# Kernel optimization log

Hardware: AMD Instinct MI355X
Metric: run time of the kernel (lower is better)

## Reference

```python
import jax, jax.numpy as jnp
import numpy as np
import math

N_EMBD = 1024
N_HEAD = 16
HEAD_DIM = N_EMBD // N_HEAD
SCALE = 1.0 / math.sqrt(HEAD_DIM)


def setup_inputs() -> dict:
    key = jax.random.key(0)
    ks = jax.random.split(key, 5)
    B, S = 1, 4096
    std = 0.02
    x = jax.random.normal(ks[0], (B, S, N_EMBD), dtype=jnp.float32)
    # Linear weights stored as [in, out] (transposed vs torch storage; same math)
    w_qkv = jax.random.normal(ks[1], (N_EMBD, 3 * N_EMBD), dtype=jnp.float32) * std
    b_qkv = jnp.zeros((3 * N_EMBD,), dtype=jnp.float32)
    w_out = jax.random.normal(ks[2], (N_EMBD, N_EMBD), dtype=jnp.float32) * std
    b_out = jnp.zeros((N_EMBD,), dtype=jnp.float32)
    return {"x": x, "w_qkv": w_qkv, "b_qkv": b_qkv, "w_out": w_out, "b_out": b_out}


def reference(x, w_qkv, b_qkv, w_out, b_out):
    B, S, D = x.shape
    qkv = x @ w_qkv + b_qkv                      # [B, S, 3D]
    q, k, v = jnp.split(qkv, 3, axis=-1)
    # [B, H, S, d]
    q = q.reshape(B, S, N_HEAD, HEAD_DIM).transpose(0, 2, 1, 3)
    k = k.reshape(B, S, N_HEAD, HEAD_DIM).transpose(0, 2, 1, 3)
    v = v.reshape(B, S, N_HEAD, HEAD_DIM).transpose(0, 2, 1, 3)
    scores = jnp.einsum("bhqd,bhkd->bhqk", q, k) * SCALE  # [B, H, S, S]
    causal = jnp.tril(jnp.ones((S, S), dtype=bool))
    scores = jnp.where(causal, scores, -jnp.inf)
    attn = jax.nn.softmax(scores, axis=-1)
    out = jnp.einsum("bhqk,bhkd->bhqd", attn, v)  # [B, H, S, d]
    out = out.transpose(0, 2, 1, 3).reshape(B, S, D)
    return out @ w_out + b_out
```

## Files before the change

### kernel.cpp

```cpp
#include <hip/hip_runtime.h>
#include <hip/hip_bf16.h>
#include <cstdint>

typedef __bf16 bf16x8 __attribute__((ext_vector_type(8)));
typedef float  f32x4  __attribute__((ext_vector_type(4)));

#define S_LEN 4096
#define D_EMB 1024
#define N3    3072
#define HDIM  64

__device__ __forceinline__ unsigned short f2bf(float f) {
    union { unsigned int i; float f; } v; v.f = f;
    unsigned int i = v.i;
    return (unsigned short)((i + 0x7FFFu + ((i >> 16) & 1u)) >> 16);
}

__device__ __forceinline__ void async16(const void* g, void* l) {
    __builtin_amdgcn_global_load_lds(
        (const __attribute__((address_space(1))) unsigned int*)g,
        (__attribute__((address_space(3))) unsigned int*)l,
        16, 0, 0);
}

__global__ void convert_f32_bf16(const float* __restrict__ src,
                                 unsigned short* __restrict__ dst, int n8) {
    const int i = blockIdx.x * blockDim.x + threadIdx.x;
    if (i >= n8) return;
    float4 f0 = *(const float4*)&src[i * 8];
    float4 f1 = *(const float4*)&src[i * 8 + 4];
    union { uint4 q; unsigned short s[8]; } o;
    o.s[0]=f2bf(f0.x); o.s[1]=f2bf(f0.y); o.s[2]=f2bf(f0.z); o.s[3]=f2bf(f0.w);
    o.s[4]=f2bf(f1.x); o.s[5]=f2bf(f1.y); o.s[6]=f2bf(f1.z); o.s[7]=f2bf(f1.w);
    *(uint4*)&dst[i * 8] = o.q;
}

__global__ void transpose_f32_to_bf16(const float* __restrict__ src,
                                      unsigned short* __restrict__ dst,
                                      int R, int ld, int c0) {
    __shared__ float tile[32][33];
    const int tx = threadIdx.x, ty = threadIdx.y;
    const int r0 = blockIdx.y * 32, cc0 = blockIdx.x * 32;
    for (int i = 0; i < 32; i += 8)
        tile[ty + i][tx] = src[(size_t)(r0 + ty + i) * ld + c0 + cc0 + tx];
    __syncthreads();
    for (int i = 0; i < 32; i += 8)
        dst[(size_t)(cc0 + ty + i) * R + r0 + tx] = f2bf(tile[tx][ty + i]);
}

__global__ void transpose_bf16(const unsigned short* __restrict__ src,
                               unsigned short* __restrict__ dst,
                               int R, int ld, int c0) {
    __shared__ unsigned short tile[32][33];
    const int tx = threadIdx.x, ty = threadIdx.y;
    const int r0 = blockIdx.y * 32, cc0 = blockIdx.x * 32;
    for (int i = 0; i < 32; i += 8)
        tile[ty + i][tx] = src[(size_t)(r0 + ty + i) * ld + c0 + cc0 + tx];
    __syncthreads();
    for (int i = 0; i < 32; i += 8)
        dst[(size_t)(cc0 + ty + i) * R + r0 + tx] = tile[tx][ty + i];
}

template <bool OUT_F32>
__global__ __launch_bounds__(256) void gemm_bt_bias(
    const unsigned short* __restrict__ A,
    const unsigned short* __restrict__ BT,
    const float* __restrict__ bias,
    void* __restrict__ Cp,
    int M, int N, int K)
{
    __shared__ __align__(16) unsigned short As[128 * 32];
    __shared__ __align__(16) unsigned short Bs[128 * 32];
    const int tid  = threadIdx.x;
    const int wave = tid >> 6, lane = tid & 63;
    const int q4 = lane >> 4, l16 = lane & 15;
    const int m0 = blockIdx.y * 128, n0 = blockIdx.x * 128;
    const int wm = (wave >> 1) * 64, wn = (wave & 1) * 64;

    f32x4 acc[4][4] = {};

    const int srow = wave * 32 + (lane >> 2);
    const int scol = (lane & 3) * 8;

    for (int k0 = 0; k0 < K; k0 += 32) {
        __syncthreads();
        for (int i = 0; i < 2; ++i) {
            const int r = srow + i * 16;
            async16(A  + (size_t)(m0 + r) * K + k0 + scol,
                    &As[(wave * 32 + i * 16) * 32 + lane * 8]);
            async16(BT + (size_t)(n0 + r) * K + k0 + scol,
                    &Bs[(wave * 32 + i * 16) * 32 + lane * 8]);
        }
        __syncthreads();

        bf16x8 af[4], bfr[4];
        for (int mi = 0; mi < 4; ++mi)
            af[mi] = *(const bf16x8*)&As[(wm + mi * 16 + l16) * 32 + q4 * 8];
        for (int ni = 0; ni < 4; ++ni)
            bfr[ni] = *(const bf16x8*)&Bs[(wn + ni * 16 + l16) * 32 + q4 * 8];
        for (int mi = 0; mi < 4; ++mi)
            for (int ni = 0; ni < 4; ++ni)
                acc[mi][ni] = __builtin_amdgcn_mfma_f32_16x16x32_bf16(
                    af[mi], bfr[ni], acc[mi][ni], 0, 0, 0);
    }

    for (int ni = 0; ni < 4; ++ni) {
        const int col = n0 + wn + ni * 16 + l16;
        const float bv = bias[col];
        for (int mi = 0; mi < 4; ++mi) {
            const int row = m0 + wm + mi * 16 + q4 * 4;
            for (int r = 0; r < 4; ++r) {
                const float val = acc[mi][ni][r] + bv;
                if constexpr (OUT_F32)
                    ((float*)Cp)[(size_t)(row + r) * N + col] = val;
                else
                    ((unsigned short*)Cp)[(size_t)(row + r) * N + col] = f2bf(val);
            }
        }
    }
}

#define LDP 72
__global__ __launch_bounds__(256) void attn_flash(
    const unsigned short* __restrict__ qkv,
    const unsigned short* __restrict__ Vt,
    unsigned short* __restrict__ X2)
{
    __shared__ __align__(16) unsigned short Ks[64 * LDP];
    __shared__ __align__(16) unsigned short Vs[64 * LDP];
    __shared__ __align__(16) unsigned short Ps[4 * 16 * LDP];
    const int tid  = threadIdx.x;
    const int wave = tid >> 6, lane = tid & 63;
    const int q4 = lane >> 4, l16 = lane & 15;
    const int h  = blockIdx.y;

    const int x = blockIdx.x, hg = blockIdx.y >> 2;
    int qt;
    if      (hg == 0) qt = x;
    else if (hg == 1) qt = 63 - x;
    else if (hg == 2) qt = (x + 16) & 63;
    else              qt = (47 - x) & 63;
    const int q0 = qt * 64;

    bf16x8 aq[2];
    {
        const unsigned short* qp =
            qkv + (size_t)(q0 + wave * 16 + l16) * N3 + h * HDIM + q4 * 8;
        aq[0] = *(const bf16x8*)(qp);
        aq[1] = *(const bf16x8*)(qp + 32);
    }

    float l_part[4] = {0.f, 0.f, 0.f, 0.f};
    f32x4 o[4] = {};

    const int rr = tid >> 3;
    const int cc = (tid & 7) * 8;
    const int ntile = qt + 1;

    for (int t = 0; t < ntile; ++t) {
        const int kv0 = t * 64;
        uint4 kv_a = *(const uint4*)&qkv[(size_t)(kv0 + rr)      * N3 + D_EMB + h * HDIM + cc];
        uint4 kv_b = *(const uint4*)&qkv[(size_t)(kv0 + 32 + rr) * N3 + D_EMB + h * HDIM + cc];
        uint4 vt_a = *(const uint4*)&Vt [(size_t)(h * HDIM + rr)      * S_LEN + kv0 + cc];
        uint4 vt_b = *(const uint4*)&Vt [(size_t)(h * HDIM + 32 + rr) * S_LEN + kv0 + cc];
        __syncthreads();
        *(uint4*)&Ks[rr * LDP + cc]        = kv_a;
        *(uint4*)&Ks[(32 + rr) * LDP + cc] = kv_b;
        *(uint4*)&Vs[rr * LDP + cc]        = vt_a;
        *(uint4*)&Vs[(32 + rr) * LDP + cc] = vt_b;
        __syncthreads();

        f32x4 sacc[4] = {};
        for (int kk = 0; kk < 2; ++kk)
            for (int nt = 0; nt < 4; ++nt) {
                bf16x8 b = *(const bf16x8*)&Ks[(nt * 16 + l16) * LDP + kk * 32 + q4 * 8];
                sacc[nt] = __builtin_amdgcn_mfma_f32_16x16x32_bf16(
                    aq[kk], b, sacc[nt], 0, 0, 0);
            }

        const bool lastt = (t == ntile - 1);
        for (int r = 0; r < 4; ++r) {
            const int grow = q0 + wave * 16 + q4 * 4 + r;
            for (int nt = 0; nt < 4; ++nt) {
                float e = __expf(sacc[nt][r] * 0.125f);
                if (lastt && (kv0 + nt * 16 + l16 > grow)) e = 0.f;
                l_part[r] += e;
                Ps[wave * 16 * LDP + (q4 * 4 + r) * LDP + nt * 16 + l16] = f2bf(e);
            }
        }
        __asm__ volatile("s_waitcnt lgkmcnt(0)" ::: "memory");

        for (int kk = 0; kk < 2; ++kk) {
            bf16x8 pa = *(const bf16x8*)&Ps[wave * 16 * LDP + l16 * LDP + kk * 32 + q4 * 8];
            for (int dt = 0; dt < 4; ++dt) {
                bf16x8 vb = *(const bf16x8*)&Vs[(dt * 16 + l16) * LDP + kk * 32 + q4 * 8];
                o[dt] = __builtin_amdgcn_mfma_f32_16x16x32_bf16(pa, vb, o[dt], 0, 0, 0);
            }
        }
    }

    float linv[4];
    for (int r = 0; r < 4; ++r) {
        float l = l_part[r];
        for (int off = 1; off < 16; off <<= 1)
            l += __shfl_xor(l, off, 16);
        linv[r] = 1.f / l;
    }
    for (int dt = 0; dt < 4; ++dt)
        for (int r = 0; r < 4; ++r) {
            const int row = q0 + wave * 16 + q4 * 4 + r;
            X2[(size_t)row * D_EMB + h * HDIM + dt * 16 + l16] =
                f2bf(o[dt][r] * linv[r]);
        }
}

extern "C" void kernel_launch(void* const* d_in, const int* in_sizes, int n_in,
                              void* d_out, int out_size, void* d_ws, size_t ws_size,
                              hipStream_t stream) {
    const float* x     = (const float*)d_in[0];
    const float* w_qkv = (const float*)d_in[1];
    const float* b_qkv = (const float*)d_in[2];
    const float* w_out = (const float*)d_in[3];
    const float* b_out = (const float*)d_in[4];
    float* out = (float*)d_out;

    char* ws = (char*)d_ws;
    unsigned short* qkv   = (unsigned short*)(ws);
    unsigned short* wqkvT = (unsigned short*)(ws + 25165824);
    unsigned short* woutT = (unsigned short*)(ws + 31457280);
    unsigned short* Vt    = (unsigned short*)(ws + 33554432);
    unsigned short* X2    = (unsigned short*)(ws + 41943040);
    unsigned short* Xb    = X2;

    convert_f32_bf16<<<(4096 * 1024 / 8 + 255) / 256, 256, 0, stream>>>(
        x, Xb, 4096 * 1024 / 8);

    transpose_f32_to_bf16<<<dim3(3072 / 32, 1024 / 32), dim3(32, 8), 0, stream>>>(
        w_qkv, wqkvT, 1024, 3072, 0);
    transpose_f32_to_bf16<<<dim3(1024 / 32, 1024 / 32), dim3(32, 8), 0, stream>>>(
        w_out, woutT, 1024, 1024, 0);

    gemm_bt_bias<false><<<dim3(3072 / 128, 4096 / 128), 256, 0, stream>>>(
        Xb, wqkvT, b_qkv, qkv, 4096, 3072, 1024);

    transpose_bf16<<<dim3(1024 / 32, 4096 / 32), dim3(32, 8), 0, stream>>>(
        qkv, Vt, 4096, 3072, 2048);

    attn_flash<<<dim3(64, 16), 256, 0, stream>>>(qkv, Vt, X2);

    gemm_bt_bias<true><<<dim3(1024 / 128, 4096 / 128), 256, 0, stream>>>(
        X2, woutT, b_out, out, 4096, 1024, 1024);
}
```

Before: 248.4 us.

## Split KV tiles across waves with register-resident K/V and LDS reduction

Restructures the attention kernel so each wave handles all 64 query rows of the block but only every fourth KV tile. K and V fragments are loaded straight from global memory into registers, which removes the per-tile shared-memory staging and block barriers. The four waves' partial outputs and row sums are then combined through LDS in a tree reduction. The softmax scale and log2(e) are folded into Q in the QKV GEMM epilogue so exp2f can be used directly. The cost is much higher register pressure (64 accumulators per wave, launch_bounds 256,2), unbalanced tile counts across waves for small qt, and a loss of the previous head-group query-tile reordering.

```diff
diff --git a/kernel.cpp b/kernel.cpp
--- a/kernel.cpp
+++ b/kernel.cpp
@@ -9,6 +9,7 @@
 #define D_EMB 1024
 #define N3    3072
 #define HDIM  64
+#define QSCALE 0.180336884f
 
 __device__ __forceinline__ unsigned short f2bf(float f) {
     union { unsigned int i; float f; } v; v.f = f;
@@ -61,7 +62,7 @@
         dst[(size_t)(cc0 + ty + i) * R + r0 + tx] = tile[tx][ty + i];
 }
 
-template <bool OUT_F32>
+template <bool OUT_F32, bool SCALE_Q>
 __global__ __launch_bounds__(256) void gemm_bt_bias(
     const unsigned short* __restrict__ A,
     const unsigned short* __restrict__ BT,
@@ -107,10 +108,11 @@
     for (int ni = 0; ni < 4; ++ni) {
         const int col = n0 + wn + ni * 16 + l16;
         const float bv = bias[col];
+        const float sc = (SCALE_Q && col < 1024) ? QSCALE : 1.f;
         for (int mi = 0; mi < 4; ++mi) {
             const int row = m0 + wm + mi * 16 + q4 * 4;
             for (int r = 0; r < 4; ++r) {
-                const float val = acc[mi][ni][r] + bv;
+                const float val = (acc[mi][ni][r] + bv) * sc;
                 if constexpr (OUT_F32)
                     ((float*)Cp)[(size_t)(row + r) * N + col] = val;
                 else
@@ -120,98 +122,131 @@
     }
 }
 
-#define LDP 72
-__global__ __launch_bounds__(256) void attn_flash(
+#define PLD 72
+
+__global__ __launch_bounds__(256, 2) void attn_flash(
     const unsigned short* __restrict__ qkv,
     const unsigned short* __restrict__ Vt,
     unsigned short* __restrict__ X2)
 {
-    __shared__ __align__(16) unsigned short Ks[64 * LDP];
-    __shared__ __align__(16) unsigned short Vs[64 * LDP];
-    __shared__ __align__(16) unsigned short Ps[4 * 16 * LDP];
+    __shared__ __align__(16) unsigned char lds[4 * 64 * PLD * 2];
     const int tid  = threadIdx.x;
     const int wave = tid >> 6, lane = tid & 63;
     const int q4 = lane >> 4, l16 = lane & 15;
     const int h  = blockIdx.y;
-
-    const int x = blockIdx.x, hg = blockIdx.y >> 2;
-    int qt;
-    if      (hg == 0) qt = x;
-    else if (hg == 1) qt = 63 - x;
-    else if (hg == 2) qt = (x + 16) & 63;
-    else              qt = (47 - x) & 63;
+    const int qt = 63 - blockIdx.x;
     const int q0 = qt * 64;
 
-    bf16x8 aq[2];
-    {
-        const unsigned short* qp =
-            qkv + (size_t)(q0 + wave * 16 + l16) * N3 + h * HDIM + q4 * 8;
-        aq[0] = *(const bf16x8*)(qp);
-        aq[1] = *(const bf16x8*)(qp + 32);
-    }
-
+    unsigned short* Pw = (unsigned short*)(lds + wave * (64 * PLD * 2));
+
+    bf16x8 bq[4][2];
+    for (int mi = 0; mi < 4; ++mi)
+        for (int kk = 0; kk < 2; ++kk)
+            bq[mi][kk] = *(const bf16x8*)&qkv[(size_t)(q0 + mi * 16 + l16) * N3
+                                             + h * HDIM + kk * 32 + q4 * 8];
+
+    f32x4 o[4][4] = {};
     float l_part[4] = {0.f, 0.f, 0.f, 0.f};
-    f32x4 o[4] = {};
-
-    const int rr = tid >> 3;
-    const int cc = (tid & 7) * 8;
-    const int ntile = qt + 1;
-
-    for (int t = 0; t < ntile; ++t) {
+
+    for (int t = wave; t <= qt; t += 4) {
         const int kv0 = t * 64;
-        uint4 kv_a = *(const uint4*)&qkv[(size_t)(kv0 + rr)      * N3 + D_EMB + h * HDIM + cc];
-        uint4 kv_b = *(const uint4*)&qkv[(size_t)(kv0 + 32 + rr) * N3 + D_EMB + h * HDIM + cc];
-        uint4 vt_a = *(const uint4*)&Vt [(size_t)(h * HDIM + rr)      * S_LEN + kv0 + cc];
-        uint4 vt_b = *(const uint4*)&Vt [(size_t)(h * HDIM + 32 + rr) * S_LEN + kv0 + cc];
-        __syncthreads();
-        *(uint4*)&Ks[rr * LDP + cc]        = kv_a;
-        *(uint4*)&Ks[(32 + rr) * LDP + cc] = kv_b;
-        *(uint4*)&Vs[rr * LDP + cc]        = vt_a;
-        *(uint4*)&Vs[(32 + rr) * LDP + cc] = vt_b;
-        __syncthreads();
-
-        f32x4 sacc[4] = {};
+        bf16x8 ak[4][2];
+        for (int nt = 0; nt < 4; ++nt)
+            for (int kk = 0; kk < 2; ++kk)
+                ak[nt][kk] = *(const bf16x8*)&qkv[(size_t)(kv0 + nt * 16 + l16) * N3
+                                                 + D_EMB + h * HDIM + kk * 32 + q4 * 8];
+        f32x4 s[4][4] = {};
         for (int kk = 0; kk < 2; ++kk)
+            for (int nt = 0; nt < 4; ++nt)
+                for (int mi = 0; mi < 4; ++mi)
+                    s[nt][mi] = __builtin_amdgcn_mfma_f32_16x16x32_bf16(
+                        ak[nt][kk], bq[mi][kk], s[nt][mi], 0, 0, 0);
+
+        const bool last = (t == qt);
+        for (int mi = 0; mi < 4; ++mi) {
+            const int qg = q0 + mi * 16 + l16;
             for (int nt = 0; nt < 4; ++nt) {
-                bf16x8 b = *(const bf16x8*)&Ks[(nt * 16 + l16) * LDP + kk * 32 + q4 * 8];
-                sacc[nt] = __builtin_amdgcn_mfma_f32_16x16x32_bf16(
-                    aq[kk], b, sacc[nt], 0, 0, 0);
+                unsigned int u[4];
+                for (int r = 0; r < 4; ++r) {
+                    float e = exp2f(s[nt][mi][r]);
+                    if (last && (kv0 + nt * 16 + q4 * 4 + r > qg)) e = 0.f;
+                    l_part[mi] += e;
+                    u[r] = __float_as_uint(e);
+                }
+                uint2 pk;
+                pk.x = __builtin_amdgcn_perm(u[1], u[0], 0x07060302u);
+                pk.y = __builtin_amdgcn_perm(u[3], u[2], 0x07060302u);
+                *(uint2*)&Pw[(mi * 16 + l16) * PLD + nt * 16 + q4 * 4] = pk;
             }
-
-        const bool lastt = (t == ntile - 1);
-        for (int r = 0; r < 4; ++r) {
-            const int grow = q0 + wave * 16 + q4 * 4 + r;
-            for (int nt = 0; nt < 4; ++nt) {
-                float e = __expf(sacc[nt][r] * 0.125f);
-                if (lastt && (kv0 + nt * 16 + l16 > grow)) e = 0.f;
-                l_part[r] += e;
-                Ps[wave * 16 * LDP + (q4 * 4 + r) * LDP + nt * 16 + l16] = f2bf(e);
+        }
+        __asm__ volatile("s_waitcnt lgkmcnt(0)" ::: "memory");
+
+        bf16x8 av[4][2], bp[4][2];
+        for (int od = 0; od < 4; ++od)
+            for (int kk = 0; kk < 2; ++kk)
+                av[od][kk] = *(const bf16x8*)&Vt[(size_t)(h * HDIM + od * 16 + l16) * S_LEN
+                                                + kv0 + kk * 32 + q4 * 8];
+        for (int mi = 0; mi < 4; ++mi)
+            for (int kk = 0; kk < 2; ++kk)
+                bp[mi][kk] = *(const bf16x8*)&Pw[(mi * 16 + l16) * PLD + kk * 32 + q4 * 8];
+        for (int kk = 0; kk < 2; ++kk)
+            for (int od = 0; od < 4; ++od)
+                for (int mi = 0; mi < 4; ++mi)
+                    o[od][mi] = __builtin_amdgcn_mfma_f32_16x16x32_bf16(
+                        av[od][kk], bp[mi][kk], o[od][mi], 0, 0, 0);
+    }
+
+    float* comb0 = (float*)lds;
+    float* comb1 = (float*)(lds + 64 * 68 * 4);
+    __syncthreads();
+    if (wave & 1) {
+        float* dst = (wave == 1) ? comb0 : comb1;
+        for (int od = 0; od < 4; ++od)
+            for (int mi = 0; mi < 4; ++mi)
+                *(f32x4*)&dst[lane * 68 + (od * 4 + mi) * 4] = o[od][mi];
+        f32x4 lv; for (int i = 0; i < 4; ++i) lv[i] = l_part[i];
+        *(f32x4*)&dst[lane * 68 + 64] = lv;
+    }
+    __syncthreads();
+    if (!(wave & 1)) {
+        const float* src = (wave == 0) ? comb0 : comb1;
+        for (int od = 0; od < 4; ++od)
+            for (int mi = 0; mi < 4; ++mi)
+                o[od][mi] += *(const f32x4*)&src[lane * 68 + (od * 4 + mi) * 4];
+        f32x4 lv = *(const f32x4*)&src[lane * 68 + 64];
+        for (int i = 0; i < 4; ++i) l_part[i] += lv[i];
+    }
+    __syncthreads();
+    if (wave == 2) {
+        for (int od = 0; od < 4; ++od)
+            for (int mi = 0; mi < 4; ++mi)
+                *(f32x4*)&comb0[lane * 68 + (od * 4 + mi) * 4] = o[od][mi];
+        f32x4 lv; for (int i = 0; i < 4; ++i) lv[i] = l_part[i];
+        *(f32x4*)&comb0[lane * 68 + 64] = lv;
+    }
+    __syncthreads();
+    if (wave == 0) {
+        for (int od = 0; od < 4; ++od)
+            for (int mi = 0; mi < 4; ++mi)
+                o[od][mi] += *(const f32x4*)&comb0[lane * 68 + (od * 4 + mi) * 4];
+        f32x4 lv = *(const f32x4*)&comb0[lane * 68 + 64];
+        float linv[4];
+        for (int mi = 0; mi < 4; ++mi) {
+            float l = l_part[mi] + lv[mi];
+            l += __shfl_xor(l, 16);
+            l += __shfl_xor(l, 32);
+            linv[mi] = 1.f / l;
+        }
+        for (int mi = 0; mi < 4; ++mi) {
+            const int q = q0 + mi * 16 + l16;
+            for (int od = 0; od < 4; ++od) {
+                union { uint2 u; unsigned short s2[4]; } pk;
+                for (int r = 0; r < 4; ++r)
+                    pk.s2[r] = f2bf(o[od][mi][r] * linv[mi]);
+                *(uint2*)&X2[(size_t)q * D_EMB + h * HDIM + od * 16 + q4 * 4] = pk.u;
             }
         }
-        __asm__ volatile("s_waitcnt lgkmcnt(0)" ::: "memory");
-
-        for (int kk = 0; kk < 2; ++kk) {
-            bf16x8 pa = *(const bf16x8*)&Ps[wave * 16 * LDP + l16 * LDP + kk * 32 + q4 * 8];
-            for (int dt = 0; dt < 4; ++dt) {
-                bf16x8 vb = *(const bf16x8*)&Vs[(dt * 16 + l16) * LDP + kk * 32 + q4 * 8];
-                o[dt] = __builtin_amdgcn_mfma_f32_16x16x32_bf16(pa, vb, o[dt], 0, 0, 0);
-            }
-        }
-    }
-
-    float linv[4];
-    for (int r = 0; r < 4; ++r) {
-        float l = l_part[r];
-        for (int off = 1; off < 16; off <<= 1)
-            l += __shfl_xor(l, off, 16);
-        linv[r] = 1.f / l;
-    }
-    for (int dt = 0; dt < 4; ++dt)
-        for (int r = 0; r < 4; ++r) {
-            const int row = q0 + wave * 16 + q4 * 4 + r;
-            X2[(size_t)row * D_EMB + h * HDIM + dt * 16 + l16] =
-                f2bf(o[dt][r] * linv[r]);
-        }
+    }
 }
 
 extern "C" void kernel_launch(void* const* d_in, const int* in_sizes, int n_in,
@@ -240,7 +275,7 @@
     transpose_f32_to_bf16<<<dim3(1024 / 32, 1024 / 32), dim3(32, 8), 0, stream>>>(
         w_out, woutT, 1024, 1024, 0);
 
-    gemm_bt_bias<false><<<dim3(3072 / 128, 4096 / 128), 256, 0, stream>>>(
+    gemm_bt_bias<false, true><<<dim3(3072 / 128, 4096 / 128), 256, 0, stream>>>(
         Xb, wqkvT, b_qkv, qkv, 4096, 3072, 1024);
 
     transpose_bf16<<<dim3(1024 / 32, 4096 / 32), dim3(32, 8), 0, stream>>>(
@@ -248,6 +283,6 @@
 
     attn_flash<<<dim3(64, 16), 256, 0, stream>>>(qkv, Vt, X2);
 
-    gemm_bt_bias<true><<<dim3(1024 / 128, 4096 / 128), 256, 0, stream>>>(
+    gemm_bt_bias<true, false><<<dim3(1024 / 128, 4096 / 128), 256, 0, stream>>>(
         X2, woutT, b_out, out, 4096, 1024, 1024);
 }
```

Result: slower. 333.5 us (+34.3%).
